# Kernel optimization log

Hardware: AMD Instinct MI355X
Metric: run time of the kernel (lower is better)

The kernel has to match this reference:

```python
import jax, jax.numpy as jnp
import numpy as np

IN_DIM = 512
HID = 256
SAMPLE = 8
TAU = 0.5
LAMBDA = 1.0
NUM_MLP = 3


def l2norm(x, axis=-1, eps=1e-12):
    n = jnp.sqrt(jnp.sum(x * x, axis=axis, keepdims=True))
    return x / jnp.maximum(n, eps)


def graphconv(adj, x, W, b):
    # GraphConv: aggregate then linear transform
    return adj @ (x @ W) + b


def mlp(x, Ws, bs):
    h = x
    for i in range(len(Ws) - 1):
        h = jax.nn.relu(h @ Ws[i] + bs[i])
    return h @ Ws[-1] + bs[-1]


def setup_inputs() -> dict:
    key = jax.random.key(0)
    ks = jax.random.split(key, 24)
    N = 16384
    # sparse-ish row-normalized adjacency surrogate (dense storage)
    a1 = jax.random.uniform(ks[0], (N, N), jnp.float32)
    a1 = (a1 > 0.999).astype(jnp.float32)
    adj1 = a1 / jnp.maximum(a1.sum(1, keepdims=True), 1.0)
    a2 = jax.random.uniform(ks[1], (N, N), jnp.float32)
    a2 = (a2 > 0.999).astype(jnp.float32)
    adj2 = a2 / jnp.maximum(a2.sum(1, keepdims=True), 1.0)
    x1 = jax.random.normal(ks[2], (N, IN_DIM), jnp.float32)
    x2 = jax.random.normal(ks[3], (N, IN_DIM), jnp.float32)
    neighbor_idx = jax.random.randint(ks[4], (N, SAMPLE), 0, N)
    neg_idx = jax.random.randint(ks[5], (N, SAMPLE), 0, N)

    def lin(k, fi, fo):
        k1, k2 = jax.random.split(k)
        s = 1.0 / np.sqrt(fi)
        return (jax.random.uniform(k1, (fi, fo), jnp.float32, -s, s),
                jax.random.uniform(k2, (fo,), jnp.float32, -s, s))

    W1, b1 = lin(ks[6], IN_DIM, HID)
    W2, b2 = lin(ks[7], HID, HID)
    tW1, tb1 = lin(ks[8], IN_DIM, HID)
    tW2, tb2 = lin(ks[9], HID, HID)
    projW, projB, semW, semB = [], [], [], []
    for i in range(NUM_MLP):
        w, b = lin(ks[10 + i], HID, HID)
        projW.append(w); projB.append(b)
        w, b = lin(ks[14 + i], HID, HID)
        semW.append(w); semB.append(b)
    return dict(adj1=adj1, adj2=adj2, x1=x1, x2=x2,
                neighbor_idx=neighbor_idx, neg_idx=neg_idx,
                W1=W1, b1=b1, W2=W2, b2=b2,
                tW1=tW1, tb1=tb1, tW2=tW2, tb2=tb2,
                projW0=projW[0], projB0=projB[0], projW1=projW[1], projB1=projB[1], projW2=projW[2], projB2=projB[2],
                semW0=semW[0], semB0=semB[0], semW1=semW[1], semB1=semB[1], semW2=semW[2], semB2=semB[2])


def contrastive_loss(projected_emd, v_emd, samp_u, samp_neg_v):
    # projected_emd, v_emd: [N,1,D]; samp_u, samp_neg_v: [N,S,D]
    pos = jnp.exp(jnp.einsum('nod,nsd->ns', projected_emd, samp_u) / TAU)  # [N,S]
    neg_sum = jnp.sum(jnp.exp(jnp.einsum('nod,nsd->ns', v_emd, samp_neg_v) / TAU), axis=1)  # [N]
    neg_score = jnp.sum(jnp.log(pos + neg_sum[:, None]), axis=1)  # [N]
    pos_score = jnp.sum(jnp.log(pos), axis=1)
    total = jnp.sum(LAMBDA * neg_score - pos_score)
    return total / samp_u.shape[0] / samp_u.shape[1]


def semi_loss(z1, z2):
    z1n = l2norm(z1); z2n = l2norm(z2)
    refl = jnp.exp((z1n @ z1n.T) / TAU)      # [N,N]
    between = jnp.exp((z1n @ z2n.T) / TAU)   # [N,N]
    return -jnp.log(jnp.diagonal(between) / (refl.sum(1) + between.sum(1) - jnp.diagonal(refl)))


def reference(adj1, adj2, x1, x2, neighbor_idx, neg_idx,
              W1, b1, W2, b2, tW1, tb1, tW2, tb2,
              projW0, projB0, projW1, projB1, projW2, projB2,
              semW0, semB0, semW1, semB1, semW2, semB2):
    pW = [projW0, projW1, projW2]; pB = [projB0, projB1, projB2]
    sW = [semW0, semW1, semW2]; sB = [semB0, semB1, semB2]
    h1 = graphconv(adj1, x1, W1, b1)
    h2 = graphconv(adj1, x2, W1, b1)
    h3 = graphconv(adj2, graphconv(adj2, x1, W1, b1), W2, b2)  # v_emd
    u_emd = l2norm(graphconv(adj2, graphconv(adj2, x1, tW1, tb1), tW2, tb2))
    projected = l2norm(mlp(h3, pW, pB))
    h1_proj = l2norm(mlp(h1, sW, sB))
    h2_proj = l2norm(mlp(h2, sW, sB))

    v_norm = l2norm(h3)
    samp_u = u_emd[neighbor_idx]          # [N,S,D]
    samp_neg_v = v_norm[neg_idx]          # [N,S,D]
    gacl = contrastive_loss(projected[:, None, :], v_norm[:, None, :], samp_u, samp_neg_v)

    l1 = semi_loss(h1_proj, h2_proj)
    l2 = semi_loss(h2_proj, h1_proj)
    sem = jnp.mean((l1 + l2) * 0.5)

    total = gacl + 0.6 * sem
    return total, gacl, sem, h3
```

## Files before the change

### kernel.cpp

```cpp
#include <hip/hip_runtime.h>
#include <hip/hip_bf16.h>

#define NN   16384
#define IND  512
#define HID  256
#define SAMP 8
#define CAP  64

typedef __bf16 bf16;
typedef __bf16 bf16x4 __attribute__((ext_vector_type(4)));
typedef __bf16 bf16x8 __attribute__((ext_vector_type(8)));
typedef float  f32x4  __attribute__((ext_vector_type(4)));

#define LOG2E_2 2.8853900817779268f

__global__ void cvt_x(const float* __restrict__ a, bf16* __restrict__ oa,
                      const float* __restrict__ b, bf16* __restrict__ ob) {
  const float* src = blockIdx.y ? b : a;
  bf16* dst = blockIdx.y ? ob : oa;
  int stride = gridDim.x * blockDim.x;
  for (int i = blockIdx.x * blockDim.x + threadIdx.x; i < (NN * IND) / 4; i += stride) {
    float4 v = ((const float4*)src)[i];
    bf16x4 o = {(bf16)v.x, (bf16)v.y, (bf16)v.z, (bf16)v.w};
    *(bf16x4*)(dst + (size_t)i * 4) = o;
  }
}

struct WtArgs {
  const float* src[10];
  bf16* dst[10];
  int K[10];
};

__global__ void cvt_weights(WtArgs a) {
  int w = blockIdx.y;
  int K = a.K[w];
  int total = K * HID;
  const float* s = a.src[w];
  bf16* d = a.dst[w];
  for (int i = blockIdx.x * blockDim.x + threadIdx.x; i < total; i += gridDim.x * blockDim.x) {
    int k = i >> 8, n = i & 255;
    d[n * K + k] = (bf16)s[i];
  }
}

__global__ void scan_adj(const float* __restrict__ adj, int* __restrict__ cols,
                         int* __restrict__ cnt) {
  int r = blockIdx.x;
  __shared__ int c;
  if (threadIdx.x == 0) c = 0;
  __syncthreads();
  const float4* row = (const float4*)(adj + (size_t)r * NN);
  int* rc = cols + (size_t)r * CAP;
  for (int i = threadIdx.x; i < NN / 4; i += blockDim.x) {
    float4 v = row[i];
    if (v.x != 0.f || v.y != 0.f || v.z != 0.f || v.w != 0.f) {
      if (v.x != 0.f) { int p = atomicAdd(&c, 1); if (p < CAP) rc[p] = 4 * i; }
      if (v.y != 0.f) { int p = atomicAdd(&c, 1); if (p < CAP) rc[p] = 4 * i + 1; }
      if (v.z != 0.f) { int p = atomicAdd(&c, 1); if (p < CAP) rc[p] = 4 * i + 2; }
      if (v.w != 0.f) { int p = atomicAdd(&c, 1); if (p < CAP) rc[p] = 4 * i + 3; }
    }
  }
  __syncthreads();
  if (threadIdx.x == 0) cnt[r] = (c < CAP) ? c : CAP;
}

__global__ void spmm(const int* __restrict__ cols, const int* __restrict__ cnt,
                     const float* __restrict__ X, const float* __restrict__ bias,
                     float* __restrict__ outF, bf16* __restrict__ outB) {
  int wid = threadIdx.x >> 6, lane = threadIdx.x & 63;
  int r = blockIdx.x * 4 + wid;
  int c = cnt[r];
  float val = 1.0f / (float)(c > 0 ? c : 1);
  const int* rc = cols + (size_t)r * CAP;
  float ax = 0.f, ay = 0.f, az = 0.f, aw = 0.f;
  for (int t = 0; t < c; ++t) {
    int col = rc[t];
    float4 v = ((const float4*)(X + (size_t)col * HID))[lane];
    ax += v.x; ay += v.y; az += v.z; aw += v.w;
  }
  float4 b4 = ((const float4*)bias)[lane];
  ax = ax * val + b4.x; ay = ay * val + b4.y; az = az * val + b4.z; aw = aw * val + b4.w;
  if (outF) {
    float* o = outF + (size_t)r * HID + lane * 4;
    o[0] = ax; o[1] = ay; o[2] = az; o[3] = aw;
  }
  if (outB) {
    bf16x4 ob = {(bf16)ax, (bf16)ay, (bf16)az, (bf16)aw};
    *(bf16x4*)(outB + (size_t)r * HID + lane * 4) = ob;
  }
}

__global__ __launch_bounds__(256) void gemm_bt(
    const bf16* __restrict__ A, const bf16* __restrict__ Bt,
    const float* __restrict__ bias, float* __restrict__ Cf, bf16* __restrict__ Cb,
    int K, int relu) {
  __shared__ bf16 As[128][72];
  __shared__ bf16 Bs[128][72];
  int m0 = blockIdx.x * 128, n0 = blockIdx.y * 128;
  int tid = threadIdx.x, wid = tid >> 6, lane = tid & 63;
  int wm = wid >> 1, wn = wid & 1, q = lane >> 4, li = lane & 15;
  f32x4 acc[4][4] = {};
  for (int k0 = 0; k0 < K; k0 += 64) {
    __syncthreads();
    #pragma unroll
    for (int ch = tid; ch < 1024; ch += 256) {
      int row = ch >> 3, kc = ch & 7;
      *(uint4*)(&As[row][kc * 8]) = *(const uint4*)(A + (size_t)(m0 + row) * K + k0 + kc * 8);
    }
    #pragma unroll
    for (int ch = tid; ch < 1024; ch += 256) {
      int row = ch >> 3, kc = ch & 7;
      *(uint4*)(&Bs[row][kc * 8]) = *(const uint4*)(Bt + (size_t)(n0 + row) * K + k0 + kc * 8);
    }
    __syncthreads();
    #pragma unroll
    for (int kk = 0; kk < 64; kk += 32) {
      bf16x8 af[4], bfr[4];
      #pragma unroll
      for (int im = 0; im < 4; ++im) af[im] = *(const bf16x8*)(&As[wm * 64 + im * 16 + li][kk + q * 8]);
      #pragma unroll
      for (int in = 0; in < 4; ++in) bfr[in] = *(const bf16x8*)(&Bs[wn * 64 + in * 16 + li][kk + q * 8]);
      #pragma unroll
      for (int im = 0; im < 4; ++im)
        #pragma unroll
        for (int in = 0; in < 4; ++in)
          acc[im][in] = __builtin_amdgcn_mfma_f32_16x16x32_bf16(af[im], bfr[in], acc[im][in], 0, 0, 0);
    }
  }
  #pragma unroll
  for (int im = 0; im < 4; ++im) {
    int grow0 = m0 + wm * 64 + im * 16 + q * 4;
    #pragma unroll
    for (int in = 0; in < 4; ++in) {
      int gcol = n0 + wn * 64 + in * 16 + li;
      float bv = bias ? bias[gcol] : 0.f;
      #pragma unroll
      for (int reg = 0; reg < 4; ++reg) {
        float v = acc[im][in][reg] + bv;
        if (relu) v = fmaxf(v, 0.f);
        size_t idx = (size_t)(grow0 + reg) * HID + gcol;
        if (Cf) Cf[idx] = v;
        if (Cb) Cb[idx] = (bf16)v;
      }
    }
  }
}

__global__ __launch_bounds__(256) void flash_sem(
    const bf16* __restrict__ P, const bf16* __restrict__ Q,
    float* __restrict__ Ra, float* __restrict__ Rb,
    float* __restrict__ Cr, float* __restrict__ Cc) {
  __shared__ bf16 As[128][72];
  __shared__ bf16 Bs[128][72];
  const bf16 *X, *Y;
  float* rowacc;
  float* colacc = nullptr;
  if (blockIdx.z == 0)      { X = P; Y = P; rowacc = Ra; }
  else if (blockIdx.z == 1) { X = Q; Y = Q; rowacc = Rb; }
  else                      { X = P; Y = Q; rowacc = Cr; colacc = Cc; }
  int bid = blockIdx.y * 128 + blockIdx.x;
  int grp = bid >> 8, loc = bid & 255;
  int bx = (grp & 7) * 16 + (loc & 15);
  int by = (grp >> 3) * 16 + (loc >> 4);
  int m0 = bx * 128, n0 = by * 128;
  int tid = threadIdx.x, wid = tid >> 6, lane = tid & 63;
  int wm = wid >> 1, wn = wid & 1, q = lane >> 4, li = lane & 15;
  f32x4 acc[4][4] = {};
  for (int k0 = 0; k0 < HID; k0 += 64) {
    __syncthreads();
    #pragma unroll
    for (int ch = tid; ch < 1024; ch += 256) {
      int row = ch >> 3, kc = ch & 7;
      *(uint4*)(&As[row][kc * 8]) = *(const uint4*)(X + (size_t)(m0 + row) * HID + k0 + kc * 8);
    }
    #pragma unroll
    for (int ch = tid; ch < 1024; ch += 256) {
      int row = ch >> 3, kc = ch & 7;
      *(uint4*)(&Bs[row][kc * 8]) = *(const uint4*)(Y + (size_t)(n0 + row) * HID + k0 + kc * 8);
    }
    __syncthreads();
    #pragma unroll
    for (int kk = 0; kk < 64; kk += 32) {
      bf16x8 af[4], bfr[4];
      #pragma unroll
      for (int im = 0; im < 4; ++im) af[im] = *(const bf16x8*)(&As[wm * 64 + im * 16 + li][kk + q * 8]);
      #pragma unroll
      for (int in = 0; in < 4; ++in) bfr[in] = *(const bf16x8*)(&Bs[wn * 64 + in * 16 + li][kk + q * 8]);
      #pragma unroll
      for (int im = 0; im < 4; ++im)
        #pragma unroll
        for (int in = 0; in < 4; ++in)
          acc[im][in] = __builtin_amdgcn_mfma_f32_16x16x32_bf16(af[im], bfr[in], acc[im][in], 0, 0, 0);
    }
  }
  float cs[4] = {0.f, 0.f, 0.f, 0.f};
  #pragma unroll
  for (int im = 0; im < 4; ++im) {
    #pragma unroll
    for (int reg = 0; reg < 4; ++reg) {
      float rs = 0.f;
      #pragma unroll
      for (int in = 0; in < 4; ++in) {
        float e = exp2f(acc[im][in][reg] * LOG2E_2);
        rs += e;
        cs[in] += e;
      }
      rs += __shfl_xor(rs, 1); rs += __shfl_xor(rs, 2);
      rs += __shfl_xor(rs, 4); rs += __shfl_xor(rs, 8);
      if (li == 0) atomicAdd(&rowacc[m0 + wm * 64 + im * 16 + q * 4 + reg], rs);
    }
  }
  if (colacc) {
    #pragma unroll
    for (int in = 0; in < 4; ++in) {
      float v = cs[in];
      v += __shfl_xor(v, 16); v += __shfl_xor(v, 32);
      if (q == 0) atomicAdd(&colacc[n0 + wn * 64 + in * 16 + li], v);
    }
  }
}

__global__ void l2norm_k(const float* __restrict__ X, float* __restrict__ outF,
                         bf16* __restrict__ outB) {
  int wid = threadIdx.x >> 6, lane = threadIdx.x & 63;
  int r = blockIdx.x * 4 + wid;
  const float* row = X + (size_t)r * HID + lane * 4;
  float a0 = row[0], a1 = row[1], a2 = row[2], a3 = row[3];
  float s = a0 * a0 + a1 * a1 + a2 * a2 + a3 * a3;
  #pragma unroll
  for (int off = 1; off < 64; off <<= 1) s += __shfl_xor(s, off);
  float inv = 1.0f / fmaxf(sqrtf(s), 1e-12f);
  a0 *= inv; a1 *= inv; a2 *= inv; a3 *= inv;
  if (outF) {
    float* o = outF + (size_t)r * HID + lane * 4;
    o[0] = a0; o[1] = a1; o[2] = a2; o[3] = a3;
  }
  if (outB) {
    bf16x4 b = {(bf16)a0, (bf16)a1, (bf16)a2, (bf16)a3};
    *(bf16x4*)(outB + (size_t)r * HID + lane * 4) = b;
  }
}

__global__ void contrast_k(const float* __restrict__ proj, const float* __restrict__ vn,
                           const float* __restrict__ ue, const int* __restrict__ nbr,
                           const int* __restrict__ neg, float* __restrict__ gsum) {
  int wid = threadIdx.x >> 6, lane = threadIdx.x & 63;
  int n = blockIdx.x * 4 + wid;
  float4 p = ((const float4*)(proj + (size_t)n * HID))[lane];
  float4 v = ((const float4*)(vn + (size_t)n * HID))[lane];
  float du[SAMP], dn[SAMP];
  for (int s = 0; s < SAMP; ++s) {
    int iu = nbr[n * SAMP + s];
    float4 u = ((const float4*)(ue + (size_t)iu * HID))[lane];
    float d = p.x * u.x + p.y * u.y + p.z * u.z + p.w * u.w;
    #pragma unroll
    for (int off = 1; off < 64; off <<= 1) d += __shfl_xor(d, off);
    du[s] = d;
    int iv = neg[n * SAMP + s];
    float4 w = ((const float4*)(vn + (size_t)iv * HID))[lane];
    float d2 = v.x * w.x + v.y * w.y + v.z * w.z + v.w * w.w;
    #pragma unroll
    for (int off = 1; off < 64; off <<= 1) d2 += __shfl_xor(d2, off);
    dn[s] = d2;
  }
  float negsum = 0.f;
  for (int s = 0; s < SAMP; ++s) negsum += expf(2.f * dn[s]);
  float ns = 0.f, ps = 0.f;
  for (int s = 0; s < SAMP; ++s) {
    float pl = 2.f * du[s];
    ns += logf(expf(pl) + negsum);
    ps += pl;
  }
  if (lane == 0) atomicAdd(gsum, ns - ps);
}

__global__ void sem_fin(const float* __restrict__ P, const float* __restrict__ Q2,
                        const float* __restrict__ Ra, const float* __restrict__ Rb,
                        const float* __restrict__ Cr, const float* __restrict__ Cc,
                        float* __restrict__ ssum) {
  int wid = threadIdx.x >> 6, lane = threadIdx.x & 63;
  int i = blockIdx.x * 4 + wid;
  float4 a = ((const float4*)(P + (size_t)i * HID))[lane];
  float4 b = ((const float4*)(Q2 + (size_t)i * HID))[lane];
  float d = a.x * b.x + a.y * b.y + a.z * b.z + a.w * b.w;
  #pragma unroll
  for (int off = 1; off < 64; off <<= 1) d += __shfl_xor(d, off);
  float db = expf(2.f * d);
  float e2 = expf(2.f);
  float l1 = -logf(db / (Ra[i] + Cr[i] - e2));
  float l2 = -logf(db / (Rb[i] + Cc[i] - e2));
  if (lane == 0) atomicAdd(ssum, 0.5f * (l1 + l2));
}

__global__ void final_k(const float* __restrict__ sums, float* __restrict__ out) {
  float gacl = sums[0] / (float)(NN * SAMP);
  float sem = sums[1] / (float)NN;
  out[0] = gacl + 0.6f * sem;
  out[1] = gacl;
  out[2] = sem;
}

extern "C" void kernel_launch(void* const* d_in, const int* in_sizes, int n_in,
                              void* d_out, int out_size, void* d_ws, size_t ws_size,
                              hipStream_t stream) {
  (void)in_sizes; (void)n_in; (void)out_size; (void)ws_size;
  const float* adj1 = (const float*)d_in[0];
  const float* adj2 = (const float*)d_in[1];
  const float* x1 = (const float*)d_in[2];
  const float* x2 = (const float*)d_in[3];
  const int* nbr = (const int*)d_in[4];
  const int* neg = (const int*)d_in[5];
  const float* W1 = (const float*)d_in[6];
  const float* b1 = (const float*)d_in[7];
  const float* W2 = (const float*)d_in[8];
  const float* b2 = (const float*)d_in[9];
  const float* tW1 = (const float*)d_in[10];
  const float* tb1 = (const float*)d_in[11];
  const float* tW2 = (const float*)d_in[12];
  const float* tb2 = (const float*)d_in[13];
  const float* pB[3] = {(const float*)d_in[15], (const float*)d_in[17], (const float*)d_in[19]};
  const float* sB[3] = {(const float*)d_in[21], (const float*)d_in[23], (const float*)d_in[25]};

  char* w = (char*)d_ws;
  auto alloc = [&](size_t bytes) -> char* {
    char* p = w;
    w += (bytes + 255) & ~(size_t)255;
    return p;
  };
  float* Ra = (float*)alloc((size_t)NN * 4);
  float* Rb = (float*)alloc((size_t)NN * 4);
  float* Cr = (float*)alloc((size_t)NN * 4);
  float* Cc = (float*)alloc((size_t)NN * 4);
  float* sums = (float*)alloc(256);
  size_t accBytes = (size_t)(w - (char*)d_ws);

  int* c1cols = (int*)alloc((size_t)NN * CAP * 4);
  int* c1cnt = (int*)alloc((size_t)NN * 4);
  int* c2cols = (int*)alloc((size_t)NN * CAP * 4);
  int* c2cnt = (int*)alloc((size_t)NN * 4);
  bf16* x1b = (bf16*)alloc((size_t)NN * IND * 2);
  bf16* x2b = (bf16*)alloc((size_t)NN * IND * 2);
  bf16* W1t = (bf16*)alloc((size_t)IND * HID * 2);
  bf16* tW1t = (bf16*)alloc((size_t)IND * HID * 2);
  bf16* W2t = (bf16*)alloc((size_t)HID * HID * 2);
  bf16* tW2t = (bf16*)alloc((size_t)HID * HID * 2);
  bf16* pWt[3], *sWt[3];
  for (int i = 0; i < 3; ++i) pWt[i] = (bf16*)alloc((size_t)HID * HID * 2);
  for (int i = 0; i < 3; ++i) sWt[i] = (bf16*)alloc((size_t)HID * HID * 2);
  const size_t FB = (size_t)NN * HID * 4;
  float* xw1 = (float*)alloc(FB);
  float* xw2 = (float*)alloc(FB);
  float* xt1 = (float*)alloc(FB);
  float* u_pre = (float*)alloc(FB);
  float* mlp_out = (float*)alloc(FB);
  float* projected = (float*)alloc(FB);
  float* h1p = (float*)alloc(FB);
  float* h2p = (float*)alloc(FB);
  float* v_norm = (float*)alloc(FB);
  float* gw = xw2;
  float* utw = xt1;
  float* u_emd = xw1;
  const size_t BB = (size_t)NN * HID * 2;
  bf16* h1b = (bf16*)alloc(BB);
  bf16* h2b = (bf16*)alloc(BB);
  bf16* gb = (bf16*)alloc(BB);
  bf16* h3b = (bf16*)alloc(BB);
  bf16* utb = (bf16*)alloc(BB);
  bf16* mA = (bf16*)alloc(BB);
  bf16* mB = (bf16*)alloc(BB);
  bf16* Pb = gb;
  bf16* Qb = utb;

  hipMemsetAsync(d_ws, 0, accBytes, stream);

  WtArgs wa;
  const float* wsrc[10] = {W1, tW1, W2, tW2,
                           (const float*)d_in[14], (const float*)d_in[16], (const float*)d_in[18],
                           (const float*)d_in[20], (const float*)d_in[22], (const float*)d_in[24]};
  bf16* wdst[10] = {W1t, tW1t, W2t, tW2t, pWt[0], pWt[1], pWt[2], sWt[0], sWt[1], sWt[2]};
  int wk[10] = {IND, IND, HID, HID, HID, HID, HID, HID, HID, HID};
  for (int i = 0; i < 10; ++i) { wa.src[i] = wsrc[i]; wa.dst[i] = wdst[i]; wa.K[i] = wk[i]; }
  cvt_weights<<<dim3(512, 10), 256, 0, stream>>>(wa);
  cvt_x<<<dim3(2048, 2), 256, 0, stream>>>(x1, x1b, x2, x2b);
  scan_adj<<<NN, 256, 0, stream>>>(adj1, c1cols, c1cnt);
  scan_adj<<<NN, 256, 0, stream>>>(adj2, c2cols, c2cnt);

  dim3 gg(NN / 128, HID / 128);
  gemm_bt<<<gg, 256, 0, stream>>>(x1b, W1t, nullptr, xw1, nullptr, IND, 0);
  gemm_bt<<<gg, 256, 0, stream>>>(x2b, W1t, nullptr, xw2, nullptr, IND, 0);
  gemm_bt<<<gg, 256, 0, stream>>>(x1b, tW1t, nullptr, xt1, nullptr, IND, 0);

  spmm<<<NN / 4, 256, 0, stream>>>(c1cols, c1cnt, xw1, b1, nullptr, h1b);
  spmm<<<NN / 4, 256, 0, stream>>>(c1cols, c1cnt, xw2, b1, nullptr, h2b);
  spmm<<<NN / 4, 256, 0, stream>>>(c2cols, c2cnt, xw1, b1, nullptr, gb);
  spmm<<<NN / 4, 256, 0, stream>>>(c2cols, c2cnt, xt1, tb1, nullptr, utb);

  gemm_bt<<<gg, 256, 0, stream>>>(gb, W2t, nullptr, gw, nullptr, HID, 0);
  float* h3out = ((float*)d_out) + 3;
  spmm<<<NN / 4, 256, 0, stream>>>(c2cols, c2cnt, gw, b2, h3out, h3b);

  gemm_bt<<<gg, 256, 0, stream>>>(utb, tW2t, nullptr, utw, nullptr, HID, 0);
  spmm<<<NN / 4, 256, 0, stream>>>(c2cols, c2cnt, utw, tb2, u_pre, nullptr);
  l2norm_k<<<NN / 4, 256, 0, stream>>>(u_pre, u_emd, nullptr);
  l2norm_k<<<NN / 4, 256, 0, stream>>>(h3out, v_norm, nullptr);

  gemm_bt<<<gg, 256, 0, stream>>>(h3b, pWt[0], pB[0], nullptr, mA, HID, 1);
  gemm_bt<<<gg, 256, 0, stream>>>(mA, pWt[1], pB[1], nullptr, mB, HID, 1);
  gemm_bt<<<gg, 256, 0, stream>>>(mB, pWt[2], pB[2], mlp_out, nullptr, HID, 0);
  l2norm_k<<<NN / 4, 256, 0, stream>>>(mlp_out, projected, nullptr);
  gemm_bt<<<gg, 256, 0, stream>>>(h1b, sWt[0], sB[0], nullptr, mA, HID, 1);
  gemm_bt<<<gg, 256, 0, stream>>>(mA, sWt[1], sB[1], nullptr, mB, HID, 1);
  gemm_bt<<<gg, 256, 0, stream>>>(mB, sWt[2], sB[2], mlp_out, nullptr, HID, 0);
  l2norm_k<<<NN / 4, 256, 0, stream>>>(mlp_out, h1p, Pb);
  gemm_bt<<<gg, 256, 0, stream>>>(h2b, sWt[0], sB[0], nullptr, mA, HID, 1);
  gemm_bt<<<gg, 256, 0, stream>>>(mA, sWt[1], sB[1], nullptr, mB, HID, 1);
  gemm_bt<<<gg, 256, 0, stream>>>(mB, sWt[2], sB[2], mlp_out, nullptr, HID, 0);
  l2norm_k<<<NN / 4, 256, 0, stream>>>(mlp_out, h2p, Qb);

  flash_sem<<<dim3(128, 128, 3), 256, 0, stream>>>(Pb, Qb, Ra, Rb, Cr, Cc);
  contrast_k<<<NN / 4, 256, 0, stream>>>(projected, v_norm, u_emd, nbr, neg, &sums[0]);
  sem_fin<<<NN / 4, 256, 0, stream>>>(h1p, h2p, Ra, Rb, Cr, Cc, &sums[1]);
  final_k<<<1, 1, 0, stream>>>(sums, (float*)d_out);
}
```

Before: 4.246 ms.

## Batch independent GEMM/SpMM/norm launches, exploit symmetry in sem, use direct-to-LDS loads

Independent GEMMs, SpMMs, adjacency scans and l2norms are merged into batched launches indexed by a grid dimension, so fewer, larger kernels run. The fused SpMM also computes the l2-normalised output directly, removing one intermediate buffer and two norm passes. The P·Pᵀ and Q·Qᵀ similarity blocks now skip the lower triangle and add each off-diagonal tile's contribution to both its rows and columns, roughly halving that work. GEMM tiles are loaded with global_load_lds into unpadded LDS, which avoids register staging but may bring LDS bank conflicts and reuses x1b memory as scratch.

Result: faster. 3.540 ms (-16.6%).

```diff
diff --git a/kernel.cpp b/kernel.cpp
--- a/kernel.cpp
+++ b/kernel.cpp
@@ -13,6 +13,10 @@
 typedef float  f32x4  __attribute__((ext_vector_type(4)));
 
 #define LOG2E_2 2.8853900817779268f
+
+#define GLOAD_LDS16(gptr, lptr) \
+  __builtin_amdgcn_global_load_lds((const __attribute__((address_space(1))) void*)(gptr), \
+                                   (__attribute__((address_space(3))) void*)(lptr), 16, 0, 0)
 
 __global__ void cvt_x(const float* __restrict__ a, bf16* __restrict__ oa,
                       const float* __restrict__ b, bf16* __restrict__ ob) {
@@ -44,8 +48,12 @@
   }
 }
 
-__global__ void scan_adj(const float* __restrict__ adj, int* __restrict__ cols,
-                         int* __restrict__ cnt) {
+__global__ void scan_adj(const float* __restrict__ adjA, const float* __restrict__ adjB,
+                         int* __restrict__ colsA, int* __restrict__ cntA,
+                         int* __restrict__ colsB, int* __restrict__ cntB) {
+  const float* adj = blockIdx.y ? adjB : adjA;
+  int* cols = blockIdx.y ? colsB : colsA;
+  int* cnt = blockIdx.y ? cntB : cntA;
   int r = blockIdx.x;
   __shared__ int c;
   if (threadIdx.x == 0) c = 0;
@@ -65,53 +73,69 @@
   if (threadIdx.x == 0) cnt[r] = (c < CAP) ? c : CAP;
 }
 
-__global__ void spmm(const int* __restrict__ cols, const int* __restrict__ cnt,
-                     const float* __restrict__ X, const float* __restrict__ bias,
-                     float* __restrict__ outF, bf16* __restrict__ outB) {
+struct SpmmB {
+  const int* cols[4]; const int* cnt[4]; const float* X[4]; const float* bias[4];
+  float* outF[4];
+  bf16* outB[4];
+  float* outNF[4];
+};
+__global__ void spmm_b(SpmmB s) {
+  int j = blockIdx.y;
   int wid = threadIdx.x >> 6, lane = threadIdx.x & 63;
   int r = blockIdx.x * 4 + wid;
-  int c = cnt[r];
+  int c = s.cnt[j][r];
   float val = 1.0f / (float)(c > 0 ? c : 1);
-  const int* rc = cols + (size_t)r * CAP;
+  const int* rc = s.cols[j] + (size_t)r * CAP;
+  const float* X = s.X[j];
   float ax = 0.f, ay = 0.f, az = 0.f, aw = 0.f;
   for (int t = 0; t < c; ++t) {
     int col = rc[t];
     float4 v = ((const float4*)(X + (size_t)col * HID))[lane];
     ax += v.x; ay += v.y; az += v.z; aw += v.w;
   }
-  float4 b4 = ((const float4*)bias)[lane];
+  float4 b4 = ((const float4*)s.bias[j])[lane];
   ax = ax * val + b4.x; ay = ay * val + b4.y; az = az * val + b4.z; aw = aw * val + b4.w;
-  if (outF) {
-    float* o = outF + (size_t)r * HID + lane * 4;
+  if (s.outF[j]) {
+    float* o = s.outF[j] + (size_t)r * HID + lane * 4;
     o[0] = ax; o[1] = ay; o[2] = az; o[3] = aw;
   }
-  if (outB) {
+  if (s.outB[j]) {
     bf16x4 ob = {(bf16)ax, (bf16)ay, (bf16)az, (bf16)aw};
-    *(bf16x4*)(outB + (size_t)r * HID + lane * 4) = ob;
-  }
-}
-
-__global__ __launch_bounds__(256) void gemm_bt(
-    const bf16* __restrict__ A, const bf16* __restrict__ Bt,
-    const float* __restrict__ bias, float* __restrict__ Cf, bf16* __restrict__ Cb,
-    int K, int relu) {
-  __shared__ bf16 As[128][72];
-  __shared__ bf16 Bs[128][72];
+    *(bf16x4*)(s.outB[j] + (size_t)r * HID + lane * 4) = ob;
+  }
+  if (s.outNF[j]) {
+    float ss = ax * ax + ay * ay + az * az + aw * aw;
+    #pragma unroll
+    for (int off = 1; off < 64; off <<= 1) ss += __shfl_xor(ss, off);
+    float inv = 1.0f / fmaxf(sqrtf(ss), 1e-12f);
+    float4 o = {ax * inv, ay * inv, az * inv, aw * inv};
+    ((float4*)(s.outNF[j] + (size_t)r * HID))[lane] = o;
+  }
+}
+
+struct GemmB {
+  const bf16* A[3]; const bf16* Bt[3]; const float* bias[3];
+  float* Cf[3]; bf16* Cb[3];
+};
+__global__ __launch_bounds__(256) void gemm_b(GemmB g, int K, int relu) {
+  __shared__ bf16 As[128][64];
+  __shared__ bf16 Bs[128][64];
+  int j = blockIdx.z;
+  const bf16* A = g.A[j];
+  const bf16* Bt = g.Bt[j];
   int m0 = blockIdx.x * 128, n0 = blockIdx.y * 128;
   int tid = threadIdx.x, wid = tid >> 6, lane = tid & 63;
   int wm = wid >> 1, wn = wid & 1, q = lane >> 4, li = lane & 15;
+  int r8 = lane >> 3, cc8 = lane & 7;
   f32x4 acc[4][4] = {};
   for (int k0 = 0; k0 < K; k0 += 64) {
-    __syncthreads();
-    #pragma unroll
-    for (int ch = tid; ch < 1024; ch += 256) {
-      int row = ch >> 3, kc = ch & 7;
-      *(uint4*)(&As[row][kc * 8]) = *(const uint4*)(A + (size_t)(m0 + row) * K + k0 + kc * 8);
-    }
-    #pragma unroll
-    for (int ch = tid; ch < 1024; ch += 256) {
-      int row = ch >> 3, kc = ch & 7;
-      *(uint4*)(&Bs[row][kc * 8]) = *(const uint4*)(Bt + (size_t)(n0 + row) * K + k0 + kc * 8);
+    if (k0) __syncthreads();
+    const bf16* gA = A + (size_t)(m0 + wid * 32 + r8) * K + k0 + cc8 * 8;
+    const bf16* gB = Bt + (size_t)(n0 + wid * 32 + r8) * K + k0 + cc8 * 8;
+    #pragma unroll
+    for (int jj = 0; jj < 4; ++jj) {
+      GLOAD_LDS16(gA + (size_t)jj * 8 * K, &As[wid * 32 + jj * 8][0]);
+      GLOAD_LDS16(gB + (size_t)jj * 8 * K, &Bs[wid * 32 + jj * 8][0]);
     }
     __syncthreads();
     #pragma unroll
@@ -128,6 +152,9 @@
           acc[im][in] = __builtin_amdgcn_mfma_f32_16x16x32_bf16(af[im], bfr[in], acc[im][in], 0, 0, 0);
     }
   }
+  float* Cf = g.Cf[j];
+  bf16* Cb = g.Cb[j];
+  const float* bias = g.bias[j];
   #pragma unroll
   for (int im = 0; im < 4; ++im) {
     int grow0 = m0 + wm * 64 + im * 16 + q * 4;
@@ -147,37 +174,36 @@
   }
 }
 
-__global__ __launch_bounds__(256) void flash_sem(
+__global__ __launch_bounds__(256) void flash_sem2(
     const bf16* __restrict__ P, const bf16* __restrict__ Q,
     float* __restrict__ Ra, float* __restrict__ Rb,
     float* __restrict__ Cr, float* __restrict__ Cc) {
-  __shared__ bf16 As[128][72];
-  __shared__ bf16 Bs[128][72];
-  const bf16 *X, *Y;
-  float* rowacc;
-  float* colacc = nullptr;
-  if (blockIdx.z == 0)      { X = P; Y = P; rowacc = Ra; }
-  else if (blockIdx.z == 1) { X = Q; Y = Q; rowacc = Rb; }
-  else                      { X = P; Y = Q; rowacc = Cr; colacc = Cc; }
+  __shared__ bf16 As[128][64];
+  __shared__ bf16 Bs[128][64];
+  int z = blockIdx.z;
   int bid = blockIdx.y * 128 + blockIdx.x;
   int grp = bid >> 8, loc = bid & 255;
   int bx = (grp & 7) * 16 + (loc & 15);
   int by = (grp >> 3) * 16 + (loc >> 4);
+  if (z < 2 && by < bx) return;
+  const bf16* X = (z == 1) ? Q : P;
+  const bf16* Y = (z == 0) ? P : Q;
+  float* rowacc = (z == 0) ? Ra : (z == 1) ? Rb : Cr;
+  float* colacc = (z == 2) ? Cc : rowacc;
+  bool docol = (z == 2) || (bx != by);
   int m0 = bx * 128, n0 = by * 128;
   int tid = threadIdx.x, wid = tid >> 6, lane = tid & 63;
   int wm = wid >> 1, wn = wid & 1, q = lane >> 4, li = lane & 15;
+  int r8 = lane >> 3, cc8 = lane & 7;
   f32x4 acc[4][4] = {};
   for (int k0 = 0; k0 < HID; k0 += 64) {
-    __syncthreads();
-    #pragma unroll
-    for (int ch = tid; ch < 1024; ch += 256) {
-      int row = ch >> 3, kc = ch & 7;
-      *(uint4*)(&As[row][kc * 8]) = *(const uint4*)(X + (size_t)(m0 + row) * HID + k0 + kc * 8);
-    }
-    #pragma unroll
-    for (int ch = tid; ch < 1024; ch += 256) {
-      int row = ch >> 3, kc = ch & 7;
-      *(uint4*)(&Bs[row][kc * 8]) = *(const uint4*)(Y + (size_t)(n0 + row) * HID + k0 + kc * 8);
+    if (k0) __syncthreads();
+    const bf16* gA = X + (size_t)(m0 + wid * 32 + r8) * HID + k0 + cc8 * 8;
+    const bf16* gB = Y + (size_t)(n0 + wid * 32 + r8) * HID + k0 + cc8 * 8;
+    #pragma unroll
+    for (int jj = 0; jj < 4; ++jj) {
+      GLOAD_LDS16(gA + (size_t)jj * 8 * HID, &As[wid * 32 + jj * 8][0]);
+      GLOAD_LDS16(gB + (size_t)jj * 8 * HID, &Bs[wid * 32 + jj * 8][0]);
     }
     __syncthreads();
     #pragma unroll
@@ -211,7 +237,7 @@
       if (li == 0) atomicAdd(&rowacc[m0 + wm * 64 + im * 16 + q * 4 + reg], rs);
     }
   }
-  if (colacc) {
+  if (docol) {
     #pragma unroll
     for (int in = 0; in < 4; ++in) {
       float v = cs[in];
@@ -221,24 +247,21 @@
   }
 }
 
-__global__ void l2norm_k(const float* __restrict__ X, float* __restrict__ outF,
-                         bf16* __restrict__ outB) {
+struct NormB { const float* X[3]; float* outF[3]; bf16* outB[3]; };
+__global__ void l2norm_b(NormB n) {
+  int j = blockIdx.y;
   int wid = threadIdx.x >> 6, lane = threadIdx.x & 63;
   int r = blockIdx.x * 4 + wid;
-  const float* row = X + (size_t)r * HID + lane * 4;
-  float a0 = row[0], a1 = row[1], a2 = row[2], a3 = row[3];
-  float s = a0 * a0 + a1 * a1 + a2 * a2 + a3 * a3;
+  float4 a = ((const float4*)(n.X[j] + (size_t)r * HID))[lane];
+  float s = a.x * a.x + a.y * a.y + a.z * a.z + a.w * a.w;
   #pragma unroll
   for (int off = 1; off < 64; off <<= 1) s += __shfl_xor(s, off);
   float inv = 1.0f / fmaxf(sqrtf(s), 1e-12f);
-  a0 *= inv; a1 *= inv; a2 *= inv; a3 *= inv;
-  if (outF) {
-    float* o = outF + (size_t)r * HID + lane * 4;
-    o[0] = a0; o[1] = a1; o[2] = a2; o[3] = a3;
-  }
-  if (outB) {
-    bf16x4 b = {(bf16)a0, (bf16)a1, (bf16)a2, (bf16)a3};
-    *(bf16x4*)(outB + (size_t)r * HID + lane * 4) = b;
+  a.x *= inv; a.y *= inv; a.z *= inv; a.w *= inv;
+  if (n.outF[j]) ((float4*)(n.outF[j] + (size_t)r * HID))[lane] = a;
+  if (n.outB[j]) {
+    bf16x4 b = {(bf16)a.x, (bf16)a.y, (bf16)a.z, (bf16)a.w};
+    *(bf16x4*)(n.outB[j] + (size_t)r * HID + lane * 4) = b;
   }
 }
 
@@ -352,7 +375,6 @@
   float* xw1 = (float*)alloc(FB);
   float* xw2 = (float*)alloc(FB);
   float* xt1 = (float*)alloc(FB);
-  float* u_pre = (float*)alloc(FB);
   float* mlp_out = (float*)alloc(FB);
   float* projected = (float*)alloc(FB);
   float* h1p = (float*)alloc(FB);
@@ -369,6 +391,8 @@
   bf16* utb = (bf16*)alloc(BB);
   bf16* mA = (bf16*)alloc(BB);
   bf16* mB = (bf16*)alloc(BB);
+  bf16* mB1 = x1b;
+  bf16* mB2 = x1b + (size_t)NN * HID;
   bf16* Pb = gb;
   bf16* Qb = utb;
 
@@ -383,42 +407,68 @@
   for (int i = 0; i < 10; ++i) { wa.src[i] = wsrc[i]; wa.dst[i] = wdst[i]; wa.K[i] = wk[i]; }
   cvt_weights<<<dim3(512, 10), 256, 0, stream>>>(wa);
   cvt_x<<<dim3(2048, 2), 256, 0, stream>>>(x1, x1b, x2, x2b);
-  scan_adj<<<NN, 256, 0, stream>>>(adj1, c1cols, c1cnt);
-  scan_adj<<<NN, 256, 0, stream>>>(adj2, c2cols, c2cnt);
-
-  dim3 gg(NN / 128, HID / 128);
-  gemm_bt<<<gg, 256, 0, stream>>>(x1b, W1t, nullptr, xw1, nullptr, IND, 0);
-  gemm_bt<<<gg, 256, 0, stream>>>(x2b, W1t, nullptr, xw2, nullptr, IND, 0);
-  gemm_bt<<<gg, 256, 0, stream>>>(x1b, tW1t, nullptr, xt1, nullptr, IND, 0);
-
-  spmm<<<NN / 4, 256, 0, stream>>>(c1cols, c1cnt, xw1, b1, nullptr, h1b);
-  spmm<<<NN / 4, 256, 0, stream>>>(c1cols, c1cnt, xw2, b1, nullptr, h2b);
-  spmm<<<NN / 4, 256, 0, stream>>>(c2cols, c2cnt, xw1, b1, nullptr, gb);
-  spmm<<<NN / 4, 256, 0, stream>>>(c2cols, c2cnt, xt1, tb1, nullptr, utb);
-
-  gemm_bt<<<gg, 256, 0, stream>>>(gb, W2t, nullptr, gw, nullptr, HID, 0);
+  scan_adj<<<dim3(NN, 2), 256, 0, stream>>>(adj1, adj2, c1cols, c1cnt, c2cols, c2cnt);
+
+  {
+    GemmB g = {};
+    g.A[0] = x1b; g.Bt[0] = W1t; g.Cf[0] = xw1;
+    g.A[1] = x2b; g.Bt[1] = W1t; g.Cf[1] = xw2;
+    g.A[2] = x1b; g.Bt[2] = tW1t; g.Cf[2] = xt1;
+    gemm_b<<<dim3(128, 2, 3), 256, 0, stream>>>(g, IND, 0);
+  }
+  {
+    SpmmB s = {};
+    s.cols[0] = c1cols; s.cnt[0] = c1cnt; s.X[0] = xw1; s.bias[0] = b1; s.outB[0] = h1b;
+    s.cols[1] = c1cols; s.cnt[1] = c1cnt; s.X[1] = xw2; s.bias[1] = b1; s.outB[1] = h2b;
+    s.cols[2] = c2cols; s.cnt[2] = c2cnt; s.X[2] = xw1; s.bias[2] = b1; s.outB[2] = gb;
+    s.cols[3] = c2cols; s.cnt[3] = c2cnt; s.X[3] = xt1; s.bias[3] = tb1; s.outB[3] = utb;
+    spmm_b<<<dim3(NN / 4, 4), 256, 0, stream>>>(s);
+  }
+  {
+    GemmB g = {};
+    g.A[0] = gb; g.Bt[0] = W2t; g.Cf[0] = gw;
+    g.A[1] = utb; g.Bt[1] = tW2t; g.Cf[1] = utw;
+    gemm_b<<<dim3(128, 2, 2), 256, 0, stream>>>(g, HID, 0);
+  }
   float* h3out = ((float*)d_out) + 3;
-  spmm<<<NN / 4, 256, 0, stream>>>(c2cols, c2cnt, gw, b2, h3out, h3b);
-
-  gemm_bt<<<gg, 256, 0, stream>>>(utb, tW2t, nullptr, utw, nullptr, HID, 0);
-  spmm<<<NN / 4, 256, 0, stream>>>(c2cols, c2cnt, utw, tb2, u_pre, nullptr);
-  l2norm_k<<<NN / 4, 256, 0, stream>>>(u_pre, u_emd, nullptr);
-  l2norm_k<<<NN / 4, 256, 0, stream>>>(h3out, v_norm, nullptr);
-
-  gemm_bt<<<gg, 256, 0, stream>>>(h3b, pWt[0], pB[0], nullptr, mA, HID, 1);
-  gemm_bt<<<gg, 256, 0, stream>>>(mA, pWt[1], pB[1], nullptr, mB, HID, 1);
-  gemm_bt<<<gg, 256, 0, stream>>>(mB, pWt[2], pB[2], mlp_out, nullptr, HID, 0);
-  l2norm_k<<<NN / 4, 256, 0, stream>>>(mlp_out, projected, nullptr);
-  gemm_bt<<<gg, 256, 0, stream>>>(h1b, sWt[0], sB[0], nullptr, mA, HID, 1);
-  gemm_bt<<<gg, 256, 0, stream>>>(mA, sWt[1], sB[1], nullptr, mB, HID, 1);
-  gemm_bt<<<gg, 256, 0, stream>>>(mB, sWt[2], sB[2], mlp_out, nullptr, HID, 0);
-  l2norm_k<<<NN / 4, 256, 0, stream>>>(mlp_out, h1p, Pb);
-  gemm_bt<<<gg, 256, 0, stream>>>(h2b, sWt[0], sB[0], nullptr, mA, HID, 1);
-  gemm_bt<<<gg, 256, 0, stream>>>(mA, sWt[1], sB[1], nullptr, mB, HID, 1);
-  gemm_bt<<<gg, 256, 0, stream>>>(mB, sWt[2], sB[2], mlp_out, nullptr, HID, 0);
-  l2norm_k<<<NN / 4, 256, 0, stream>>>(mlp_out, h2p, Qb);
-
-  flash_sem<<<dim3(128, 128, 3), 256, 0, stream>>>(Pb, Qb, Ra, Rb, Cr, Cc);
+  {
+    SpmmB s = {};
+    s.cols[0] = c2cols; s.cnt[0] = c2cnt; s.X[0] = gw; s.bias[0] = b2;
+    s.outF[0] = h3out; s.outB[0] = h3b; s.outNF[0] = v_norm;
+    s.cols[1] = c2cols; s.cnt[1] = c2cnt; s.X[1] = utw; s.bias[1] = tb2;
+    s.outNF[1] = u_emd;
+    spmm_b<<<dim3(NN / 4, 2), 256, 0, stream>>>(s);
+  }
+  {
+    GemmB g = {};
+    g.A[0] = h3b; g.Bt[0] = pWt[0]; g.bias[0] = pB[0]; g.Cb[0] = mA;
+    g.A[1] = h1b; g.Bt[1] = sWt[0]; g.bias[1] = sB[0]; g.Cb[1] = gb;
+    g.A[2] = h2b; g.Bt[2] = sWt[0]; g.bias[2] = sB[0]; g.Cb[2] = utb;
+    gemm_b<<<dim3(128, 2, 3), 256, 0, stream>>>(g, HID, 1);
+  }
+  {
+    GemmB g = {};
+    g.A[0] = mA; g.Bt[0] = pWt[1]; g.bias[0] = pB[1]; g.Cb[0] = mB;
+    g.A[1] = gb; g.Bt[1] = sWt[1]; g.bias[1] = sB[1]; g.Cb[1] = mB1;
+    g.A[2] = utb; g.Bt[2] = sWt[1]; g.bias[2] = sB[1]; g.Cb[2] = mB2;
+    gemm_b<<<dim3(128, 2, 3), 256, 0, stream>>>(g, HID, 1);
+  }
+  {
+    GemmB g = {};
+    g.A[0] = mB; g.Bt[0] = pWt[2]; g.bias[0] = pB[2]; g.Cf[0] = mlp_out;
+    g.A[1] = mB1; g.Bt[1] = sWt[2]; g.bias[1] = sB[2]; g.Cf[1] = xw2;
+    g.A[2] = mB2; g.Bt[2] = sWt[2]; g.bias[2] = sB[2]; g.Cf[2] = xt1;
+    gemm_b<<<dim3(128, 2, 3), 256, 0, stream>>>(g, HID, 0);
+  }
+  {
+    NormB nb2 = {};
+    nb2.X[0] = mlp_out; nb2.outF[0] = projected;
+    nb2.X[1] = xw2; nb2.outF[1] = h1p; nb2.outB[1] = Pb;
+    nb2.X[2] = xt1; nb2.outF[2] = h2p; nb2.outB[2] = Qb;
+    l2norm_b<<<dim3(NN / 4, 3), 256, 0, stream>>>(nb2);
+  }
+
+  flash_sem2<<<dim3(128, 128, 3), 256, 0, stream>>>(Pb, Qb, Ra, Rb, Cr, Cc);
   contrast_k<<<NN / 4, 256, 0, stream>>>(projected, v_norm, u_emd, nbr, neg, &sums[0]);
   sem_fin<<<NN / 4, 256, 0, stream>>>(h1p, h2p, Ra, Rb, Cr, Cc, &sums[1]);
   final_k<<<1, 1, 0, stream>>>(sums, (float*)d_out);
```
